# Performance work log

Measured on AMD Instinct MI355X. Metric: run time of the kernel, lower is better.

## Reference

```python
import math
import jax, jax.numpy as jnp
import numpy as np

B, T, H, E, K, F = 4, 4096, 512, 8, 2, 2048
CAP_FACTOR, ROUND_TO = 0.3125, 128


def _capacity(num_tokens):
    cap = math.ceil(CAP_FACTOR * num_tokens)
    cap = ROUND_TO * math.ceil(cap / ROUND_TO)
    return max(1, min(cap, num_tokens))


def setup_inputs() -> dict:
    key = jax.random.key(0)
    k0, k1, k2, k3 = jax.random.split(key, 4)
    x = jax.random.normal(k0, (B, T, H), jnp.float32)
    router_w = jax.random.normal(k1, (H, E), jnp.float32) * 0.02
    w1 = jax.random.normal(k2, (E, H, F), jnp.float32) * (1.0 / np.sqrt(H))
    b1 = jnp.zeros((E, F), jnp.float32)
    w2 = jax.random.normal(k3, (E, F, H), jnp.float32) * (1.0 / np.sqrt(F))
    b2 = jnp.zeros((E, H), jnp.float32)
    return {"x": x, "router_w": router_w, "w1": w1, "b1": b1, "w2": w2, "b2": b2}


def reference(x, router_w, w1, b1, w2, b2):
    Bc, Tc, Hc = x.shape
    n = Bc * Tc
    cap = _capacity(n)  # static: 5120
    flat = x.reshape(n, Hc)

    # Router + top-k selection (fp32 logits, softmax over selected logits)
    logits = (flat @ router_w).astype(jnp.float32)          # [n, E]
    sel_logits, expert_idx = jax.lax.top_k(logits, K)       # [n, K]
    weights = jax.nn.softmax(sel_logits, axis=-1)           # [n, K]

    # Flatten (token, k) assignments and sort by expert (stable)
    fe = expert_idx.reshape(-1).astype(jnp.int32)           # [n*K]
    fw = weights.reshape(-1)
    tok = jnp.broadcast_to(jnp.arange(n, dtype=jnp.int32)[:, None], expert_idx.shape).reshape(-1)
    order = jnp.argsort(fe)  # jax sort is stable
    se, st, sw = fe[order], tok[order], fw[order]

    # Per-expert slot index; assignments beyond capacity are dropped
    counts = jnp.bincount(se, length=E)                     # [E]
    offsets = (jnp.cumsum(counts) - counts).astype(jnp.int32)
    slot = jnp.arange(se.shape[0], dtype=jnp.int32) - offsets[se]
    keep = slot < cap
    sw = jnp.where(keep, sw, 0.0)                           # dropped tokens contribute 0

    # Pack into fixed-capacity expert buffers (out-of-range slots dropped)
    sx = flat[st]                                           # [n*K, H]
    expert_inputs = jnp.zeros((E, cap, Hc), flat.dtype).at[se, slot].set(sx, mode='drop')

    # Grouped expert MLP: Dense(F) -> GELU -> Dense(H)
    h = jax.nn.gelu(jnp.einsum('ech,ehf->ecf', expert_inputs, w1) + b1[:, None, :])
    out = jnp.einsum('ecf,efh->ech', h, w2) + b2[:, None, :]

    # Zero invalid (unused) slots
    clipped = jnp.minimum(counts, cap)
    valid = (jnp.arange(cap, dtype=jnp.int32)[None, :] < clipped[:, None])[..., None]
    out = jnp.where(valid, out, 0)

    # Scatter-combine weighted expert outputs back to tokens
    slot_c = jnp.minimum(slot, cap - 1)                     # dropped rows have weight 0
    gathered = out[se, slot_c] * sw[:, None].astype(out.dtype)
    combined = jnp.zeros((n, Hc), out.dtype).at[st].add(gathered)
    return combined.reshape(Bc, Tc, Hc)
```

## Files before the change

### kernel.cpp

```cpp
#include <hip/hip_runtime.h>
#include <hip/hip_bf16.h>

#define NTOK 16384
#define HD   512
#define ED   8
#define FD   2048
#define CAP  5120
#define NA   32768

typedef __bf16 bf16x8 __attribute__((ext_vector_type(8)));
typedef float  f32x4  __attribute__((ext_vector_type(4)));

static constexpr size_t OFF_EIDX = 0;
static constexpr size_t OFF_WGT  = 131072;
static constexpr size_t OFF_STOK = 262144;
static constexpr size_t OFF_ASLOT= 425984;
static constexpr size_t OFF_ECNT = 557056;
static constexpr size_t OFF_W2T  = 1u << 20;
static constexpr size_t OFF_H    = OFF_W2T + (size_t)ED*HD*FD*2;
static constexpr size_t OFF_W1T  = OFF_H   + (size_t)ED*CAP*FD*2;
static constexpr size_t OFF_XBF  = OFF_W1T + (size_t)ED*FD*HD*2;
static constexpr size_t OFF_EOUT = OFF_XBF + (size_t)NTOK*HD*2;

__device__ __forceinline__ unsigned short f2bf(float f) {
    __bf16 b = (__bf16)f;
    return __builtin_bit_cast(unsigned short, b);
}
__device__ __forceinline__ unsigned short f2h(float f) {
    _Float16 h = (_Float16)f;
    return __builtin_bit_cast(unsigned short, h);
}
__device__ __forceinline__ float h2f(unsigned short u) {
    return (float)__builtin_bit_cast(_Float16, u);
}

__device__ __forceinline__ float gelu_fast(float v) {
    const float t = v * v;
    const float u = v * fmaf(t, 0.0713548214f, 1.5957691216f);
    const float e = __expf(-u);
    return v * __builtin_amdgcn_rcpf(1.f + e);
}

__global__ __launch_bounds__(256) void transpose_cast_kernel(
    const float* __restrict__ in, unsigned short* __restrict__ out, int R, int C)
{
    __shared__ unsigned short tile[32][33];
    const int e = blockIdx.z;
    in  += (size_t)e * R * C;
    out += (size_t)e * R * C;
    const int r0 = blockIdx.y * 32, c0 = blockIdx.x * 32;
    const int tr = threadIdx.x >> 3, tc = (threadIdx.x & 7) * 4;
    const float4 v = *(const float4*)(in + (size_t)(r0 + tr) * C + c0 + tc);
    tile[tr][tc + 0] = f2bf(v.x);
    tile[tr][tc + 1] = f2bf(v.y);
    tile[tr][tc + 2] = f2bf(v.z);
    tile[tr][tc + 3] = f2bf(v.w);
    __syncthreads();
    ushort4 o;
    o.x = tile[tc + 0][tr]; o.y = tile[tc + 1][tr];
    o.z = tile[tc + 2][tr]; o.w = tile[tc + 3][tr];
    *(ushort4*)(out + (size_t)(c0 + tr) * R + r0 + tc) = o;
}

__global__ __launch_bounds__(256) void router_kernel(
    const float* __restrict__ x, const float* __restrict__ rw,
    int* __restrict__ eidx, float* __restrict__ wgt,
    unsigned short* __restrict__ xbf)
{
    __shared__ float rws[HD * ED];
    const int tid = threadIdx.x;
    for (int i = tid * 4; i < HD * ED; i += 256 * 4)
        *(float4*)(rws + i) = *(const float4*)(rw + i);
    __syncthreads();

    const int wid = tid >> 6, lane = tid & 63;
    const int t = blockIdx.x * 4 + wid;
    const float* xr = x + (size_t)t * HD;

    float acc[ED];
#pragma unroll
    for (int e = 0; e < ED; e++) acc[e] = 0.f;

    float4 xv0 = *(const float4*)(xr + lane * 8);
    float4 xv1 = *(const float4*)(xr + lane * 8 + 4);
    float xv[8] = {xv0.x, xv0.y, xv0.z, xv0.w, xv1.x, xv1.y, xv1.z, xv1.w};

    union { unsigned short us[8]; uint4 v; } pk;
#pragma unroll
    for (int j = 0; j < 8; j++) pk.us[j] = f2bf(xv[j]);
    *(uint4*)(xbf + (size_t)t * HD + lane * 8) = pk.v;

#pragma unroll
    for (int j = 0; j < 8; j++) {
        const int h = lane * 8 + j;
#pragma unroll
        for (int e = 0; e < ED; e++) acc[e] += xv[j] * rws[h * ED + e];
    }
#pragma unroll
    for (int off = 32; off >= 1; off >>= 1) {
#pragma unroll
        for (int e = 0; e < ED; e++) acc[e] += __shfl_down(acc[e], off);
    }
    if (lane == 0) {
        int e0 = 0; float l0 = acc[0];
        for (int e = 1; e < ED; e++) if (acc[e] > l0) { l0 = acc[e]; e0 = e; }
        int e1 = 0; float l1 = -1e30f;
        for (int e = 0; e < ED; e++) {
            if (e == e0) continue;
            if (acc[e] > l1) { l1 = acc[e]; e1 = e; }
        }
        const float ex = expf(l1 - l0);
        const float inv = 1.f / (1.f + ex);
        eidx[t * 2 + 0] = e0;  eidx[t * 2 + 1] = e1;
        wgt [t * 2 + 0] = inv; wgt [t * 2 + 1] = ex * inv;
    }
}

__global__ __launch_bounds__(1024) void scan_kernel(
    const int* __restrict__ eidx,
    int* __restrict__ stok, int* __restrict__ aslot, int* __restrict__ ecnt)
{
    __shared__ int wcnt[32][16][ED];
    __shared__ int woff[32][16][ED];
    const int tid = threadIdx.x;
    const int lane = tid & 63, wid = tid >> 6;
    const unsigned long long below = (1ull << lane) - 1ull;

    for (int i = tid; i < ED * CAP; i += 1024) stok[i] = -1;

    for (int c = 0; c < NA / 1024; c++) {
        const int e = eidx[c * 1024 + tid];
#pragma unroll
        for (int ee = 0; ee < ED; ee++) {
            unsigned long long m = __ballot(e == ee);
            if (lane == 0) wcnt[c][wid][ee] = __popcll(m);
        }
    }
    __syncthreads();

    if (wid < ED) {
        const int e = wid;
        int carry = 0;
#pragma unroll
        for (int r = 0; r < 8; r++) {
            const int idx = r * 64 + lane;
            const int v = wcnt[idx >> 4][idx & 15][e];
            int s = v;
#pragma unroll
            for (int off = 1; off < 64; off <<= 1) {
                int u = __shfl_up(s, off);
                if (lane >= off) s += u;
            }
            woff[idx >> 4][idx & 15][e] = carry + s - v;
            carry += __shfl(s, 63);
        }
        if (lane == 0) ecnt[e] = carry < CAP ? carry : CAP;
    }
    __syncthreads();

    for (int c = 0; c < NA / 1024; c++) {
        const int a = c * 1024 + tid;
        const int e = eidx[a];
        int myrank = 0;
#pragma unroll
        for (int ee = 0; ee < ED; ee++) {
            unsigned long long m = __ballot(e == ee);
            if (ee == e) myrank = __popcll(m & below);
        }
        const int slot = woff[c][wid][e] + myrank;
        if (slot < CAP) {
            stok[e * CAP + slot] = a >> 1;
            aslot[a] = slot;
        } else {
            aslot[a] = -1;
        }
    }
}

template<int KD, int ND, int NT, bool G1>
__global__ __launch_bounds__(256) void gemm_mfma(
    const unsigned short* __restrict__ Abase,
    const unsigned short* __restrict__ Bt,
    const float* __restrict__ bias,
    const int* __restrict__ stok,
    const int* __restrict__ ecnt,
    unsigned short* __restrict__ hout)
{
    constexpr int BUFE = 128 * 32;
    __shared__ __align__(16) unsigned short As[2 * BUFE];
    __shared__ __align__(16) unsigned short Bs[2 * BUFE];

    const int tid = threadIdx.x;
    const int e  = blockIdx.x & 7;
    const int g  = blockIdx.x >> 3;
    const int n0 = (g % NT) * 128;
    const int m0 = (g / NT) * 128;

    if (m0 >= ecnt[e]) return;

    const int lane = tid & 63;
    const int wid  = tid >> 6;

    const int q  = tid & 3;
    const int r1 = tid >> 2;
    const int r2 = r1 + 64;

    size_t ai1, ai2;
    if constexpr (G1) {
        const int t1 = stok[e * CAP + m0 + r1];
        const int t2 = stok[e * CAP + m0 + r2];
        ai1 = (size_t)(t1 >= 0 ? t1 : 0);
        ai2 = (size_t)(t2 >= 0 ? t2 : 0);
    } else {
        ai1 = (size_t)(e * CAP + m0 + r1);
        ai2 = (size_t)(e * CAP + m0 + r2);
    }
    const unsigned short* arow1 = Abase + ai1 * KD + q * 8;
    const unsigned short* arow2 = Abase + ai2 * KD + q * 8;
    const unsigned short* brow1 = Bt + ((size_t)e * ND + n0 + r1) * KD + q * 8;
    const unsigned short* brow2 = Bt + ((size_t)e * ND + n0 + r2) * KD + q * 8;

    const int cSw = q ^ ((r1 >> 1) & 3);
    const int oW1 = r1 * 32 + cSw * 8;
    const int oW2 = r2 * 32 + cSw * 8;

    const int wrow = (wid & 1) * 64;
    const int wcol = (wid >> 1) * 64;
    const int l15  = lane & 15;
    const int quad = lane >> 4;
    const int xq   = quad ^ ((l15 >> 1) & 3);
    const int fA   = (wrow + l15) * 32 + xq * 8;
    const int fB   = (wcol + l15) * 32 + xq * 8;

    f32x4 acc[4][4];
#pragma unroll
    for (int i = 0; i < 4; i++)
#pragma unroll
        for (int j = 0; j < 4; j++) acc[i][j] = (f32x4)0.f;

#define COMPUTE(PBUF)                                                          \
    {                                                                          \
        const unsigned short* Ab = As + (PBUF) * BUFE;                         \
        const unsigned short* Bb = Bs + (PBUF) * BUFE;                         \
        bf16x8 af[4], bfv[4];                                                  \
        _Pragma("unroll")                                                      \
        for (int i = 0; i < 4; i++) af[i]  = *(const bf16x8*)(Ab + fA + i * 512); \
        _Pragma("unroll")                                                      \
        for (int j = 0; j < 4; j++) bfv[j] = *(const bf16x8*)(Bb + fB + j * 512); \
        _Pragma("unroll")                                                      \
        for (int i = 0; i < 4; i++)                                            \
            _Pragma("unroll")                                                  \
            for (int j = 0; j < 4; j++)                                        \
                acc[i][j] = __builtin_amdgcn_mfma_f32_16x16x32_bf16(           \
                    bfv[j], af[i], acc[i][j], 0, 0, 0);                        \
    }

#define LBAR asm volatile("s_waitcnt lgkmcnt(0)\n\ts_barrier" ::: "memory")

    float4 ra1 = *(const float4*)(arow1);
    float4 ra2 = *(const float4*)(arow2);
    float4 rb1 = *(const float4*)(brow1);
    float4 rb2 = *(const float4*)(brow2);
    *(float4*)(&As[oW1]) = ra1;
    *(float4*)(&As[oW2]) = ra2;
    *(float4*)(&Bs[oW1]) = rb1;
    *(float4*)(&Bs[oW2]) = rb2;
    if (32 < KD) {
        ra1 = *(const float4*)(arow1 + 32);
        ra2 = *(const float4*)(arow2 + 32);
        rb1 = *(const float4*)(brow1 + 32);
        rb2 = *(const float4*)(brow2 + 32);
    }
    LBAR;

    int rbuf = 0;
    for (int kc = 0; kc < KD; kc += 32) {
        const int wb = (rbuf ^ 1) * BUFE;
        if (kc + 32 < KD) {
            *(float4*)(&As[wb + oW1]) = ra1;
            *(float4*)(&As[wb + oW2]) = ra2;
            *(float4*)(&Bs[wb + oW1]) = rb1;
            *(float4*)(&Bs[wb + oW2]) = rb2;
            if (kc + 64 < KD) {
                ra1 = *(const float4*)(arow1 + kc + 64);
                ra2 = *(const float4*)(arow2 + kc + 64);
                rb1 = *(const float4*)(brow1 + kc + 64);
                rb2 = *(const float4*)(brow2 + kc + 64);
            }
        }
        COMPUTE(rbuf);
        LBAR;
        rbuf ^= 1;
    }
#undef COMPUTE
#undef LBAR

#pragma unroll
    for (int i = 0; i < 4; i++) {
        unsigned short* hrow = hout
            + ((size_t)e * CAP + m0 + wrow + i * 16 + l15) * ND
            + n0 + wcol + quad * 4;
#pragma unroll
        for (int j = 0; j < 4; j++) {
            const float4 b4 = *(const float4*)(
                bias + (size_t)e * ND + n0 + wcol + j * 16 + quad * 4);
            const float v0 = acc[i][j][0] + b4.x;
            const float v1 = acc[i][j][1] + b4.y;
            const float v2 = acc[i][j][2] + b4.z;
            const float v3 = acc[i][j][3] + b4.w;
            ushort4 o;
            if constexpr (G1) {
                o.x = f2bf(gelu_fast(v0)); o.y = f2bf(gelu_fast(v1));
                o.z = f2bf(gelu_fast(v2)); o.w = f2bf(gelu_fast(v3));
            } else {
                o.x = f2h(v0); o.y = f2h(v1); o.z = f2h(v2); o.w = f2h(v3);
            }
            *(ushort4*)(hrow + j * 16) = o;
        }
    }
}

__global__ __launch_bounds__(256) void combine_kernel(
    const unsigned short* __restrict__ eout,
    const int* __restrict__ eidx, const int* __restrict__ aslot,
    const float* __restrict__ wgt, float* __restrict__ out)
{
    const int tid = threadIdx.x;
    const int t  = blockIdx.x * 2 + (tid >> 7);
    const int h0 = (tid & 127) * 4;
    float r0 = 0.f, r1 = 0.f, r2 = 0.f, r3 = 0.f;
#pragma unroll
    for (int k = 0; k < 2; k++) {
        const int a = t * 2 + k;
        const int s = aslot[a];
        if (s >= 0) {
            const float w = wgt[a];
            const int e = eidx[a];
            const ushort4 v = *(const ushort4*)(eout + ((size_t)e * CAP + s) * HD + h0);
            r0 += w * h2f(v.x); r1 += w * h2f(v.y);
            r2 += w * h2f(v.z); r3 += w * h2f(v.w);
        }
    }
    float4 o; o.x = r0; o.y = r1; o.z = r2; o.w = r3;
    *(float4*)(out + (size_t)t * HD + h0) = o;
}

extern "C" void kernel_launch(void* const* d_in, const int* in_sizes, int n_in,
                              void* d_out, int out_size, void* d_ws, size_t ws_size,
                              hipStream_t stream)
{
    const float* x  = (const float*)d_in[0];
    const float* rw = (const float*)d_in[1];
    const float* w1 = (const float*)d_in[2];
    const float* b1 = (const float*)d_in[3];
    const float* w2 = (const float*)d_in[4];
    const float* b2 = (const float*)d_in[5];
    float* out = (float*)d_out;

    char* ws = (char*)d_ws;
    int*   eidx  = (int*)  (ws + OFF_EIDX);
    float* wgt   = (float*)(ws + OFF_WGT);
    int*   stok  = (int*)  (ws + OFF_STOK);
    int*   aslot = (int*)  (ws + OFF_ASLOT);
    int*   ecnt  = (int*)  (ws + OFF_ECNT);
    unsigned short* w2t  = (unsigned short*)(ws + OFF_W2T);
    unsigned short* hbuf = (unsigned short*)(ws + OFF_H);
    unsigned short* w1t  = (unsigned short*)(ws + OFF_W1T);
    unsigned short* xbf  = (unsigned short*)(ws + OFF_XBF);
    unsigned short* eout = (unsigned short*)(ws + OFF_EOUT);

    transpose_cast_kernel<<<dim3(FD / 32, HD / 32, ED), 256, 0, stream>>>(w1, w1t, HD, FD);
    transpose_cast_kernel<<<dim3(HD / 32, FD / 32, ED), 256, 0, stream>>>(w2, w2t, FD, HD);
    router_kernel<<<NTOK / 4, 256, 0, stream>>>(x, rw, eidx, wgt, xbf);
    scan_kernel<<<1, 1024, 0, stream>>>(eidx, stok, aslot, ecnt);

    gemm_mfma<HD, FD, FD/128, true>
        <<<8 * (FD/128) * (CAP/128), 256, 0, stream>>>(
        xbf, w1t, b1, stok, ecnt, hbuf);

    gemm_mfma<FD, HD, HD/128, false>
        <<<8 * (HD/128) * (CAP/128), 256, 0, stream>>>(
        hbuf, w2t, b2, nullptr, ecnt, eout);

    combine_kernel<<<NTOK / 2, 256, 0, stream>>>(eout, eidx, aslot, wgt, out);
}
```

Measured before the change: 456.3 us.

## Enlarge GEMM M tile to 256 rows and merge weight transpose launches

The grouped expert GEMMs now use a 256x128 block tile, so each wave computes 128x64 with 8x4 MFMA accumulators. This doubles reuse of each B fragment loaded into LDS and halves the number of blocks. The two weight transpose-cast launches are merged into one launch over a padded grid, where unused blocks exit early. The larger tile raises register and LDS use, which can lower occupancy, and it gives the second GEMM fewer blocks (8*4*20) to spread across the GPU.

```diff
diff --git a/kernel.cpp b/kernel.cpp
--- a/kernel.cpp
+++ b/kernel.cpp
@@ -42,12 +42,18 @@
 }
 
 __global__ __launch_bounds__(256) void transpose_cast_kernel(
-    const float* __restrict__ in, unsigned short* __restrict__ out, int R, int C)
+    const float* __restrict__ w1, unsigned short* __restrict__ w1t,
+    const float* __restrict__ w2, unsigned short* __restrict__ w2t)
 {
     __shared__ unsigned short tile[32][33];
-    const int e = blockIdx.z;
-    in  += (size_t)e * R * C;
-    out += (size_t)e * R * C;
+    const int z = blockIdx.z;
+    const bool is1 = z < ED;
+    const int e = is1 ? z : z - ED;
+    const int R = is1 ? HD : FD;
+    const int C = is1 ? FD : HD;
+    if (blockIdx.x * 32 >= C || blockIdx.y * 32 >= R) return;
+    const float* in = (is1 ? w1 : w2) + (size_t)e * HD * FD;
+    unsigned short* out = (is1 ? w1t : w2t) + (size_t)e * HD * FD;
     const int r0 = blockIdx.y * 32, c0 = blockIdx.x * 32;
     const int tr = threadIdx.x >> 3, tc = (threadIdx.x & 7) * 4;
     const float4 v = *(const float4*)(in + (size_t)(r0 + tr) * C + c0 + tc);
@@ -186,128 +192,132 @@
     const int* __restrict__ ecnt,
     unsigned short* __restrict__ hout)
 {
-    constexpr int BUFE = 128 * 32;
-    __shared__ __align__(16) unsigned short As[2 * BUFE];
-    __shared__ __align__(16) unsigned short Bs[2 * BUFE];
+    constexpr int ABUF = 256 * 32;
+    constexpr int BBUF = 128 * 32;
+    __shared__ __align__(16) unsigned short As[2 * ABUF];
+    __shared__ __align__(16) unsigned short Bs[2 * BBUF];
 
     const int tid = threadIdx.x;
     const int e  = blockIdx.x & 7;
     const int g  = blockIdx.x >> 3;
     const int n0 = (g % NT) * 128;
-    const int m0 = (g / NT) * 128;
+    const int m0 = (g / NT) * 256;
 
     if (m0 >= ecnt[e]) return;
 
     const int lane = tid & 63;
     const int wid  = tid >> 6;
 
-    const int q  = tid & 3;
-    const int r1 = tid >> 2;
-    const int r2 = r1 + 64;
-
-    size_t ai1, ai2;
-    if constexpr (G1) {
-        const int t1 = stok[e * CAP + m0 + r1];
-        const int t2 = stok[e * CAP + m0 + r2];
-        ai1 = (size_t)(t1 >= 0 ? t1 : 0);
-        ai2 = (size_t)(t2 >= 0 ? t2 : 0);
-    } else {
-        ai1 = (size_t)(e * CAP + m0 + r1);
-        ai2 = (size_t)(e * CAP + m0 + r2);
-    }
-    const unsigned short* arow1 = Abase + ai1 * KD + q * 8;
-    const unsigned short* arow2 = Abase + ai2 * KD + q * 8;
-    const unsigned short* brow1 = Bt + ((size_t)e * ND + n0 + r1) * KD + q * 8;
-    const unsigned short* brow2 = Bt + ((size_t)e * ND + n0 + r2) * KD + q * 8;
-
-    const int cSw = q ^ ((r1 >> 1) & 3);
-    const int oW1 = r1 * 32 + cSw * 8;
-    const int oW2 = r2 * 32 + cSw * 8;
-
-    const int wrow = (wid & 1) * 64;
-    const int wcol = (wid >> 1) * 64;
+    const int q = tid & 3;
+    const int r = tid >> 2;
+
+    unsigned int aoff[4], boff[2];
+#pragma unroll
+    for (int i = 0; i < 4; i++) {
+        unsigned int arow;
+        if constexpr (G1) {
+            const int t = stok[e * CAP + m0 + r + i * 64];
+            arow = (unsigned int)(t >= 0 ? t : 0);
+        } else {
+            arow = (unsigned int)(e * CAP + m0 + r + i * 64);
+        }
+        aoff[i] = arow * KD + q * 8;
+    }
+#pragma unroll
+    for (int i = 0; i < 2; i++)
+        boff[i] = (unsigned int)((e * ND + n0 + r + i * 64) * KD) + q * 8;
+
+    const int cSw = q ^ ((r >> 1) & 3);
+    int oWa[4], oWb[2];
+#pragma unroll
+    for (int i = 0; i < 4; i++) oWa[i] = (r + i * 64) * 32 + cSw * 8;
+#pragma unroll
+    for (int i = 0; i < 2; i++) oWb[i] = (r + i * 64) * 32 + cSw * 8;
+
+    const int wm = wid >> 1, wn = wid & 1;
     const int l15  = lane & 15;
     const int quad = lane >> 4;
     const int xq   = quad ^ ((l15 >> 1) & 3);
-    const int fA   = (wrow + l15) * 32 + xq * 8;
-    const int fB   = (wcol + l15) * 32 + xq * 8;
-
-    f32x4 acc[4][4];
-#pragma unroll
-    for (int i = 0; i < 4; i++)
+    const int fA   = (wm * 128 + l15) * 32 + xq * 8;
+    const int fB   = (wn * 64 + l15) * 32 + xq * 8;
+
+    f32x4 acc[8][4];
+#pragma unroll
+    for (int i = 0; i < 8; i++)
 #pragma unroll
         for (int j = 0; j < 4; j++) acc[i][j] = (f32x4)0.f;
 
 #define COMPUTE(PBUF)                                                          \
     {                                                                          \
-        const unsigned short* Ab = As + (PBUF) * BUFE;                         \
-        const unsigned short* Bb = Bs + (PBUF) * BUFE;                         \
-        bf16x8 af[4], bfv[4];                                                  \
-        _Pragma("unroll")                                                      \
-        for (int i = 0; i < 4; i++) af[i]  = *(const bf16x8*)(Ab + fA + i * 512); \
+        const unsigned short* Ab = As + (PBUF) * ABUF;                         \
+        const unsigned short* Bb = Bs + (PBUF) * BBUF;                         \
+        bf16x8 af[8], bfv[4];                                                  \
+        _Pragma("unroll")                                                      \
+        for (int i = 0; i < 8; i++) af[i]  = *(const bf16x8*)(Ab + fA + i * 512); \
         _Pragma("unroll")                                                      \
         for (int j = 0; j < 4; j++) bfv[j] = *(const bf16x8*)(Bb + fB + j * 512); \
         _Pragma("unroll")                                                      \
-        for (int i = 0; i < 4; i++)                                            \
+        for (int i = 0; i < 8; i++)                                            \
             _Pragma("unroll")                                                  \
             for (int j = 0; j < 4; j++)                                        \
                 acc[i][j] = __builtin_amdgcn_mfma_f32_16x16x32_bf16(           \
                     bfv[j], af[i], acc[i][j], 0, 0, 0);                        \
     }
 
+#define LOADT(KC)                                                              \
+    {                                                                          \
+        _Pragma("unroll")                                                      \
+        for (int i = 0; i < 4; i++) ra[i] = *(const float4*)(Abase + aoff[i] + (KC)); \
+        _Pragma("unroll")                                                      \
+        for (int i = 0; i < 2; i++) rb[i] = *(const float4*)(Bt + boff[i] + (KC)); \
+    }
+
+#define WRITET(WB)                                                             \
+    {                                                                          \
+        _Pragma("unroll")                                                      \
+        for (int i = 0; i < 4; i++) *(float4*)(&As[(WB) * ABUF + oWa[i]]) = ra[i]; \
+        _Pragma("unroll")                                                      \
+        for (int i = 0; i < 2; i++) *(float4*)(&Bs[(WB) * BBUF + oWb[i]]) = rb[i]; \
+    }
+
 #define LBAR asm volatile("s_waitcnt lgkmcnt(0)\n\ts_barrier" ::: "memory")
 
-    float4 ra1 = *(const float4*)(arow1);
-    float4 ra2 = *(const float4*)(arow2);
-    float4 rb1 = *(const float4*)(brow1);
-    float4 rb2 = *(const float4*)(brow2);
-    *(float4*)(&As[oW1]) = ra1;
-    *(float4*)(&As[oW2]) = ra2;
-    *(float4*)(&Bs[oW1]) = rb1;
-    *(float4*)(&Bs[oW2]) = rb2;
-    if (32 < KD) {
-        ra1 = *(const float4*)(arow1 + 32);
-        ra2 = *(const float4*)(arow2 + 32);
-        rb1 = *(const float4*)(brow1 + 32);
-        rb2 = *(const float4*)(brow2 + 32);
-    }
+    float4 ra[4], rb[2];
+    LOADT(0);
+    WRITET(0);
+    LOADT(32);
     LBAR;
 
     int rbuf = 0;
     for (int kc = 0; kc < KD; kc += 32) {
-        const int wb = (rbuf ^ 1) * BUFE;
         if (kc + 32 < KD) {
-            *(float4*)(&As[wb + oW1]) = ra1;
-            *(float4*)(&As[wb + oW2]) = ra2;
-            *(float4*)(&Bs[wb + oW1]) = rb1;
-            *(float4*)(&Bs[wb + oW2]) = rb2;
-            if (kc + 64 < KD) {
-                ra1 = *(const float4*)(arow1 + kc + 64);
-                ra2 = *(const float4*)(arow2 + kc + 64);
-                rb1 = *(const float4*)(brow1 + kc + 64);
-                rb2 = *(const float4*)(brow2 + kc + 64);
-            }
+            WRITET(rbuf ^ 1);
+            if (kc + 64 < KD) LOADT(kc + 64);
         }
         COMPUTE(rbuf);
         LBAR;
         rbuf ^= 1;
     }
 #undef COMPUTE
+#undef LOADT
+#undef WRITET
 #undef LBAR
 
-#pragma unroll
-    for (int i = 0; i < 4; i++) {
+    float4 b4[4];
+#pragma unroll
+    for (int j = 0; j < 4; j++)
+        b4[j] = *(const float4*)(bias + (size_t)e * ND + n0 + wn * 64 + j * 16 + quad * 4);
+#pragma unroll
+    for (int i = 0; i < 8; i++) {
         unsigned short* hrow = hout
-            + ((size_t)e * CAP + m0 + wrow + i * 16 + l15) * ND
-            + n0 + wcol + quad * 4;
+            + ((size_t)e * CAP + m0 + wm * 128 + i * 16 + l15) * ND
+            + n0 + wn * 64 + quad * 4;
 #pragma unroll
         for (int j = 0; j < 4; j++) {
-            const float4 b4 = *(const float4*)(
-                bias + (size_t)e * ND + n0 + wcol + j * 16 + quad * 4);
-            const float v0 = acc[i][j][0] + b4.x;
-            const float v1 = acc[i][j][1] + b4.y;
-            const float v2 = acc[i][j][2] + b4.z;
-            const float v3 = acc[i][j][3] + b4.w;
+            const float v0 = acc[i][j][0] + b4[j].x;
+            const float v1 = acc[i][j][1] + b4[j].y;
+            const float v2 = acc[i][j][2] + b4[j].z;
+            const float v3 = acc[i][j][3] + b4[j].w;
             ushort4 o;
             if constexpr (G1) {
                 o.x = f2bf(gelu_fast(v0)); o.y = f2bf(gelu_fast(v1));
@@ -369,17 +379,17 @@
     unsigned short* xbf  = (unsigned short*)(ws + OFF_XBF);
     unsigned short* eout = (unsigned short*)(ws + OFF_EOUT);
 
-    transpose_cast_kernel<<<dim3(FD / 32, HD / 32, ED), 256, 0, stream>>>(w1, w1t, HD, FD);
-    transpose_cast_kernel<<<dim3(HD / 32, FD / 32, ED), 256, 0, stream>>>(w2, w2t, FD, HD);
+    transpose_cast_kernel<<<dim3(FD / 32, FD / 32, 2 * ED), 256, 0, stream>>>(
+        w1, w1t, w2, w2t);
     router_kernel<<<NTOK / 4, 256, 0, stream>>>(x, rw, eidx, wgt, xbf);
     scan_kernel<<<1, 1024, 0, stream>>>(eidx, stok, aslot, ecnt);
 
     gemm_mfma<HD, FD, FD/128, true>
-        <<<8 * (FD/128) * (CAP/128), 256, 0, stream>>>(
+        <<<8 * (FD/128) * (CAP/256), 256, 0, stream>>>(
         xbf, w1t, b1, stok, ecnt, hbuf);
 
     gemm_mfma<FD, HD, HD/128, false>
-        <<<8 * (HD/128) * (CAP/128), 256, 0, stream>>>(
+        <<<8 * (HD/128) * (CAP/256), 256, 0, stream>>>(
         hbuf, w2t, b2, nullptr, ecnt, eout);
 
     combine_kernel<<<NTOK / 2, 256, 0, stream>>>(eout, eidx, aslot, wgt, out);
```

After: 886.2 us. 1.94x slower.
